# Optimization experiments

Measured on AMD Instinct MI355X. Metric: run time of the kernel, lower is better.

Reference implementation:

```python
import jax, jax.numpy as jnp
import numpy as np

B, T, C, H = 4, 2048, 1024, 16
D = C // H


def setup_inputs() -> dict:
    key = jax.random.key(0)
    ks = jax.random.split(key, 5)
    s = C ** -0.5  # keep linear outputs O(1) like standard init
    x = jax.random.normal(ks[0], (B, T, C), dtype=jnp.float32)
    Wq = jax.random.normal(ks[1], (C, C), dtype=jnp.float32) * s
    Wk = jax.random.normal(ks[2], (C, C), dtype=jnp.float32) * s
    Wv = jax.random.normal(ks[3], (C, C), dtype=jnp.float32) * s
    Wproj = jax.random.normal(ks[4], (C, C), dtype=jnp.float32) * s
    alpha_raw = jnp.zeros((1, H, 1, 1), dtype=jnp.float32)
    beta_raw = jnp.zeros((1, H, 1, 1), dtype=jnp.float32)
    state = jnp.zeros((B, H, D, D), dtype=jnp.float32)
    return dict(x=x, Wq=Wq, Wk=Wk, Wv=Wv, Wproj=Wproj,
                alpha_raw=alpha_raw, beta_raw=beta_raw, state=state)


def reference(x, Wq, Wk, Wv, Wproj, alpha_raw, beta_raw, state):
    Bx, Tx, Cx = x.shape
    Hn = alpha_raw.shape[1]
    Dh = Cx // Hn
    # projections (torch Linear: x @ W^T), split heads -> (B, H, T, D)
    def proj(W):
        return (x @ W.T).reshape(Bx, Tx, Hn, Dh).transpose(0, 2, 1, 3)
    q, k, v = proj(Wq), proj(Wk), proj(Wv)
    # F.normalize(k, dim=-1) with eps=1e-12
    k = k / jnp.maximum(jnp.linalg.norm(k, axis=-1, keepdims=True), 1e-12)
    alpha = jax.nn.sigmoid(alpha_raw) * 0.5  # (1, H, 1, 1)
    beta = jax.nn.sigmoid(beta_raw) * 0.5

    def step(st, qkv):
        qt, kt, vt = qkv  # each (B, H, D)
        # y_t = q_t @ state^T
        y = jnp.einsum('bhe,bhde->bhd', qt, st)
        # Mk = state @ k_t
        Mk = jnp.einsum('bhde,bhe->bhd', st, kt)
        st = st - alpha * jnp.einsum('bhd,bhe->bhde', Mk, kt) \
                + beta * jnp.einsum('bhd,bhe->bhde', vt, kt)
        return st, y

    # scan over time: (T, B, H, D)
    qT = q.transpose(2, 0, 1, 3)
    kT = k.transpose(2, 0, 1, 3)
    vT = v.transpose(2, 0, 1, 3)
    state_f, ys = jax.lax.scan(step, state, (qT, kT, vT))
    y = ys.transpose(1, 0, 2, 3).reshape(Bx, Tx, Cx)  # (B, T, C)
    out = y @ Wproj.T
    return out, state_f
```

## Files before the change

kernel.cpp:

```cpp
#include <hip/hip_runtime.h>
#include <hip/hip_bf16.h>
#include <cstdint>

#define B_ 4
#define T_ 2048
#define C_ 1024
#define H_ 16
#define D_ 64
#define NC_ 32
#define L_ 64

typedef __attribute__((ext_vector_type(8))) short bf16x8;
typedef __attribute__((ext_vector_type(4))) float f32x4;

static __device__ __forceinline__ unsigned short f2bf(float f) {
  unsigned u = __float_as_uint(f);
  u += 0x7fff + ((u >> 16) & 1);
  return (unsigned short)(u >> 16);
}
static __device__ __forceinline__ float bf2f(unsigned short b) {
  return __uint_as_float(((unsigned)b) << 16);
}
static __device__ __forceinline__ int swz128(int row, int byte) {
  return row * 128 + (byte ^ ((row & 7) << 4));
}

#define LDS_BARRIER() asm volatile("s_waitcnt lgkmcnt(0)\ns_barrier" ::: "memory")

__global__ __launch_bounds__(256) void cvt_kernel(const float* __restrict__ src,
                                                  unsigned short* __restrict__ dst, int n) {
  int i = (blockIdx.x * 256 + threadIdx.x) * 4;
  if (i >= n) return;
  float4 v = *reinterpret_cast<const float4*>(src + i);
  ushort4 o;
  o.x = f2bf(v.x); o.y = f2bf(v.y); o.z = f2bf(v.z); o.w = f2bf(v.w);
  *reinterpret_cast<ushort4*>(dst + i) = o;
}

__global__ __launch_bounds__(256) void cvt_w_kernel(const float* __restrict__ wq,
                                                    const float* __restrict__ wk,
                                                    const float* __restrict__ wv,
                                                    const float* __restrict__ wp,
                                                    unsigned short* __restrict__ W3,
                                                    unsigned short* __restrict__ Wp) {
  const int g = blockIdx.x >> 10;
  const float* src = (g == 0) ? wq : (g == 1) ? wk : (g == 2) ? wv : wp;
  unsigned short* dst = (g < 3) ? (W3 + (long)g * 1048576) : Wp;
  int i = ((blockIdx.x & 1023) * 256 + threadIdx.x) * 4;
  float4 v = *reinterpret_cast<const float4*>(src + i);
  ushort4 o;
  o.x = f2bf(v.x); o.y = f2bf(v.y); o.z = f2bf(v.z); o.w = f2bf(v.w);
  *reinterpret_cast<ushort4*>(dst + i) = o;
}

#define STAGE256(GP, GR0, KT, LOFF) do {                                          \
    const unsigned short* _s = (GP) + ((GR0) + wid * 8 + lr8) * 1024L             \
                               + (long)(KT) * 64 + skb * 8;                       \
    char* _d = (char*)lds + (LOFF) + wid * 1024;                                  \
    __builtin_amdgcn_global_load_lds((const __attribute__((address_space(1))) void*)_s,      \
        (__attribute__((address_space(3))) void*)_d, 16, 0, 0);                   \
    __builtin_amdgcn_global_load_lds((const __attribute__((address_space(1))) void*)(_s + 64 * 1024L), \
        (__attribute__((address_space(3))) void*)(_d + 8192), 16, 0, 0);          \
  } while (0)

#define PHASE256(AO, BO, MH, NH, STG) do {                                        \
    asm volatile("s_waitcnt vmcnt(6)" ::: "memory");                              \
    bf16x8 av[4][2], bv[2][2];                                                    \
    {                                                                             \
      const char* ab = (const char*)lds + (AO) + (MH) * 16384 + arow;             \
      const char* bb = (const char*)lds + (BO) + (NH) * 16384 + brow;             \
      _Pragma("unroll")                                                           \
      for (int j = 0; j < 4; ++j) {                                               \
        av[j][0] = *(const bf16x8*)(ab + j * 4096 + cb0);                         \
        av[j][1] = *(const bf16x8*)(ab + j * 4096 + cb1);                         \
      }                                                                           \
      _Pragma("unroll")                                                           \
      for (int j2 = 0; j2 < 2; ++j2) {                                            \
        bv[j2][0] = *(const bf16x8*)(bb + j2 * 8192 + cb0);                       \
        bv[j2][1] = *(const bf16x8*)(bb + j2 * 8192 + cb1);                       \
      }                                                                           \
    }                                                                             \
    STG;                                                                          \
    __builtin_amdgcn_s_barrier();                                                 \
    asm volatile("s_waitcnt lgkmcnt(0)" ::: "memory");                            \
    __builtin_amdgcn_sched_barrier(0);                                            \
    __builtin_amdgcn_s_setprio(1);                                                \
    _Pragma("unroll")                                                             \
    for (int j = 0; j < 4; ++j)                                                   \
      _Pragma("unroll")                                                           \
      for (int j2 = 0; j2 < 2; ++j2)                                              \
        acc[(MH) * 4 + j][(NH) * 2 + j2] = __builtin_amdgcn_mfma_f32_16x16x32_bf16( \
            av[j][0], bv[j2][0], acc[(MH) * 4 + j][(NH) * 2 + j2], 0, 0, 0);      \
    _Pragma("unroll")                                                             \
    for (int j = 0; j < 4; ++j)                                                   \
      _Pragma("unroll")                                                           \
      for (int j2 = 0; j2 < 2; ++j2)                                              \
        acc[(MH) * 4 + j][(NH) * 2 + j2] = __builtin_amdgcn_mfma_f32_16x16x32_bf16( \
            av[j][1], bv[j2][1], acc[(MH) * 4 + j][(NH) * 2 + j2], 0, 0, 0);      \
    __builtin_amdgcn_s_setprio(0);                                                \
    __builtin_amdgcn_s_barrier();                                                 \
  } while (0)

__global__ __launch_bounds__(512, 2) void gemm256_bt(
    const unsigned short* __restrict__ A,
    const unsigned short* __restrict__ Bw,
    unsigned short* __restrict__ C, int N) {
  __shared__ __align__(16) char lds[131072];
  enum { EA = 0, EB = 32768, OA = 65536, OB = 98304, HF = 16384 };
  const int tid = threadIdx.x;
  const int wid = tid >> 6, lane = tid & 63;
  const int wm = wid >> 2, wn = wid & 3;
  const int f = lane & 15, g = lane >> 4;
  const int lr8 = lane >> 3, lc = lane & 7;
  const int skb = lc ^ lr8;
  const int bid = blockIdx.y * gridDim.x + blockIdx.x;
  const int cpx = (gridDim.x * gridDim.y) >> 3;
  const int sw = (bid & 7) * cpx + (bid >> 3);
  const long bM = (long)(sw / gridDim.x) * 256;
  const long bN = (long)(sw % gridDim.x) * 256;
  const int cb0 = ((0 + g) ^ (f & 7)) * 16;
  const int cb1 = ((4 + g) ^ (f & 7)) * 16;
  const int arow = (wm * 16 + f) * 128;
  const int brow = (wn * 16 + f) * 128;

  f32x4 acc[8][4] = {};

  STAGE256(A, bM, 0, EA);
  STAGE256(Bw, bN, 0, EB);
  STAGE256(A, bM + 128, 0, EA + HF);
  STAGE256(Bw, bN + 128, 0, EB + HF);
  STAGE256(Bw, bN, 1, OB);
  STAGE256(A, bM, 1, OA);
  asm volatile("s_waitcnt vmcnt(8)" ::: "memory");
  __builtin_amdgcn_s_barrier();

  for (int i = 0; i < 8; ++i) {
    const int todd = 2 * i + 1;
    int te = 2 * i + 2; if (te > 14) te = 14;
    int to = 2 * i + 3; if (to > 15) to = 15;
    PHASE256(EA, EB, 0, 0, STAGE256(A, bM + 128, todd, OA + HF));
    PHASE256(EA, EB, 1, 0, STAGE256(Bw, bN + 128, todd, OB + HF));
    PHASE256(EA, EB, 0, 1, STAGE256(Bw, bN, te, EB));
    PHASE256(EA, EB, 1, 1, STAGE256(A, bM, te, EA));
    PHASE256(OA, OB, 0, 0, STAGE256(A, bM + 128, te, EA + HF));
    PHASE256(OA, OB, 1, 0, STAGE256(Bw, bN + 128, te, EB + HF));
    PHASE256(OA, OB, 0, 1, STAGE256(Bw, bN, to, OB));
    PHASE256(OA, OB, 1, 1, STAGE256(A, bM, to, OA));
  }

#pragma unroll
  for (int mf = 0; mf < 8; ++mf) {
    long row = bM + (mf >> 2) * 128 + (mf & 3) * 32 + wm * 16 + g * 4;
#pragma unroll
    for (int nf = 0; nf < 4; ++nf) {
      long col = bN + (nf >> 1) * 128 + (nf & 1) * 64 + wn * 16 + f;
#pragma unroll
      for (int r = 0; r < 4; ++r)
        C[(row + r) * (long)N + col] = f2bf(acc[mf][nf][r]);
    }
  }
}

template<int OUT_BF16>
__global__ __launch_bounds__(256) void gemm_bt(const unsigned short* __restrict__ A,
                                               const unsigned short* __restrict__ Bw,
                                               void* __restrict__ Cp,
                                               int M, int N, int K) {
  __shared__ __align__(16) unsigned short sA[128 * 32];
  __shared__ __align__(16) unsigned short sB[128 * 32];
  const int tid = threadIdx.x;
  const int wid = tid >> 6, lane = tid & 63;
  const int wm = wid >> 1, wn = wid & 1;
  const int bid = blockIdx.y * gridDim.x + blockIdx.x;
  const int cpx = (gridDim.x * gridDim.y) >> 3;
  const int sw = (bid & 7) * cpx + (bid >> 3);
  const long blockM = (long)(sw / gridDim.x) * 128;
  const long blockN = (long)(sw % gridDim.x) * 128;

  f32x4 acc[4][4] = {};

  const int ar = lane >> 2;
  const int ac = (lane & 3) * 8;
  const unsigned short* Abase = A + (blockM + wid * 32 + ar) * (long)K + ac;
  const unsigned short* Bbase = Bw + (blockN + wid * 32 + ar) * (long)K + ac;
  char* sAb = (char*)sA + wid * 2048;
  char* sBb = (char*)sB + wid * 2048;

  for (int k0 = 0; k0 < K; k0 += 32) {
    __syncthreads();
    __builtin_amdgcn_global_load_lds((const __attribute__((address_space(1))) void*)(Abase + k0),
                                     (__attribute__((address_space(3))) void*)(sAb), 16, 0, 0);
    __builtin_amdgcn_global_load_lds((const __attribute__((address_space(1))) void*)(Abase + 16 * (long)K + k0),
                                     (__attribute__((address_space(3))) void*)(sAb + 1024), 16, 0, 0);
    __builtin_amdgcn_global_load_lds((const __attribute__((address_space(1))) void*)(Bbase + k0),
                                     (__attribute__((address_space(3))) void*)(sBb), 16, 0, 0);
    __builtin_amdgcn_global_load_lds((const __attribute__((address_space(1))) void*)(Bbase + 16 * (long)K + k0),
                                     (__attribute__((address_space(3))) void*)(sBb + 1024), 16, 0, 0);
    __syncthreads();

    const int koff = (lane >> 4) * 8;
    const int rA = wm * 64 + (lane & 15);
    const int rB = wn * 64 + (lane & 15);
    bf16x8 af[4], bfr[4];
#pragma unroll
    for (int m = 0; m < 4; ++m)
      af[m] = *reinterpret_cast<const bf16x8*>(&sA[(rA + m * 16) * 32 + koff]);
#pragma unroll
    for (int n = 0; n < 4; ++n)
      bfr[n] = *reinterpret_cast<const bf16x8*>(&sB[(rB + n * 16) * 32 + koff]);
#pragma unroll
    for (int m = 0; m < 4; ++m)
#pragma unroll
      for (int n = 0; n < 4; ++n)
        acc[m][n] = __builtin_amdgcn_mfma_f32_16x16x32_bf16(af[m], bfr[n], acc[m][n], 0, 0, 0);
  }

  const int cr = (lane >> 4) * 4;
  const int cc = lane & 15;
#pragma unroll
  for (int m = 0; m < 4; ++m) {
    long R = blockM + wm * 64 + m * 16 + cr;
#pragma unroll
    for (int n = 0; n < 4; ++n) {
      long Cc = blockN + wn * 64 + n * 16 + cc;
#pragma unroll
      for (int r = 0; r < 4; ++r) {
        if (OUT_BF16)
          ((unsigned short*)Cp)[(R + r) * (long)N + Cc] = f2bf(acc[m][n][r]);
        else
          ((float*)Cp)[(R + r) * (long)N + Cc] = acc[m][n][r];
      }
    }
  }
}

__global__ __launch_bounds__(256) void chunk_prep(
    unsigned short* __restrict__ qkv,
    const float* __restrict__ a_raw, const float* __restrict__ b_raw,
    unsigned short* __restrict__ Ubuf, unsigned short* __restrict__ Wbuf,
    unsigned short* __restrict__ SLbuf) {
  __shared__ __align__(16) unsigned short sK[64 * 64];
  __shared__ __align__(16) unsigned short sQ[64 * 64];
  __shared__ __align__(16) unsigned short sV[64 * 64];
  __shared__ float sA[64 * 64];

  const int blk = blockIdx.x;
  const int bh = blk >> 5, c = blk & 31;
  const int b = bh >> 4, h = bh & 15;
  const int tid = threadIdx.x;
  const int wid = tid >> 6, lane = tid & 63;

  const float alpha = 0.5f / (1.f + __expf(-a_raw[h]));
  const float beta  = 0.5f / (1.f + __expf(-b_raw[h]));

  {
    const int row = tid >> 2, cg = tid & 3;
    unsigned short* gp = qkv + (long)(b * 2048 + c * 64 + row) * 3072 + h * 64 + cg * 16;
    bf16x8 q0 = *(const bf16x8*)(gp);
    bf16x8 q1 = *(const bf16x8*)(gp + 8);
    bf16x8 k0 = *(const bf16x8*)(gp + 1024);
    bf16x8 k1 = *(const bf16x8*)(gp + 1024 + 8);
    bf16x8 v0 = *(const bf16x8*)(gp + 2048);
    bf16x8 v1 = *(const bf16x8*)(gp + 2048 + 8);
    float kf[16];
    float ss = 0.f;
#pragma unroll
    for (int i = 0; i < 8; ++i) { kf[i] = bf2f((unsigned short)k0[i]); ss += kf[i] * kf[i]; }
#pragma unroll
    for (int i = 0; i < 8; ++i) { kf[8 + i] = bf2f((unsigned short)k1[i]); ss += kf[8 + i] * kf[8 + i]; }
    ss += __shfl_xor(ss, 1);
    ss += __shfl_xor(ss, 2);
    const float inv = 1.f / fmaxf(sqrtf(ss), 1e-12f);
    bf16x8 n0, n1;
#pragma unroll
    for (int i = 0; i < 8; ++i) { n0[i] = (short)f2bf(kf[i] * inv); n1[i] = (short)f2bf(kf[8 + i] * inv); }
    *(bf16x8*)((char*)sK + swz128(row, cg * 32)) = n0;
    *(bf16x8*)((char*)sK + swz128(row, cg * 32 + 16)) = n1;
    *(bf16x8*)((char*)sQ + swz128(row, cg * 32)) = q0;
    *(bf16x8*)((char*)sQ + swz128(row, cg * 32 + 16)) = q1;
    *(bf16x8*)((char*)sV + row * 128 + cg * 32) = v0;
    *(bf16x8*)((char*)sV + row * 128 + cg * 32 + 16) = v1;
  }
  __syncthreads();

  {
    const int erow = tid >> 2, tq = tid & 3;
    unsigned short kt[16];
#pragma unroll
    for (int i = 0; i < 16; ++i)
      kt[i] = *(const unsigned short*)((const char*)sK + swz128(tq * 16 + i, 2 * erow));
    unsigned short* vp = qkv + (long)(b * 2048 + c * 64 + erow) * 3072 + 2048 + h * 64 + tq * 16;
    *(bf16x8*)vp = *(const bf16x8*)kt;
    *(bf16x8*)(vp + 8) = *(const bf16x8*)(kt + 8);
  }

  const int rfrag = lane & 15, koff = (lane >> 4) * 8, crow = (lane >> 4) * 4;
  const int w2 = wid & 1;
  if (wid < 2) {
#pragma unroll
    for (int mt = 0; mt < 2; ++mt) {
      const int m = w2 * 2 + mt;
      const int ra = 16 * m + rfrag;
      f32x4 acc[4] = {};
#pragma unroll
      for (int ks = 0; ks < 2; ++ks) {
        bf16x8 af = *(const bf16x8*)((const char*)sK + swz128(ra, ks * 64 + koff * 2));
#pragma unroll
        for (int n = 0; n < 4; ++n) {
          bf16x8 bf = *(const bf16x8*)((const char*)sK + swz128(16 * n + rfrag, ks * 64 + koff * 2));
          acc[n] = __builtin_amdgcn_mfma_f32_16x16x32_bf16(af, bf, acc[n], 0, 0, 0);
        }
      }
#pragma unroll
      for (int n = 0; n < 4; ++n)
#pragma unroll
        for (int r = 0; r < 4; ++r)
          sA[(16 * m + crow + r) * 64 + 16 * n + rfrag] = acc[n][r];
    }
  } else {
#pragma unroll
    for (int mt = 0; mt < 2; ++mt) {
      const int m = w2 * 2 + mt;
      const int ra = 16 * m + rfrag;
      f32x4 acc[4] = {};
#pragma unroll
      for (int ks = 0; ks < 2; ++ks) {
        bf16x8 af = *(const bf16x8*)((const char*)sQ + swz128(ra, ks * 64 + koff * 2));
#pragma unroll
        for (int n = 0; n < 4; ++n) {
          bf16x8 bf = *(const bf16x8*)((const char*)sK + swz128(16 * n + rfrag, ks * 64 + koff * 2));
          acc[n] = __builtin_amdgcn_mfma_f32_16x16x32_bf16(af, bf, acc[n], 0, 0, 0);
        }
      }
#pragma unroll
      for (int n = 0; n < 4; ++n)
#pragma unroll
        for (int r = 0; r < 4; ++r) {
          int t = 16 * m + crow + r, j = 16 * n + rfrag;
          SLbuf[(long)blk * 4096 + t * 64 + j] = (j < t) ? f2bf(acc[n][r]) : (unsigned short)0;
        }
    }
  }
  __syncthreads();

  if (wid < 2) {
    const int d = lane;
    float x[64];
#pragma unroll
    for (int t = 0; t < 64; ++t) {
      float rhs;
      if (wid == 0) rhs = beta * bf2f(sV[t * 64 + d]);
      else          rhs = alpha * bf2f(*(const unsigned short*)((const char*)sK + swz128(t, 2 * d)));
      float s = 0.f;
#pragma unroll
      for (int j = 0; j < t; ++j) s = fmaf(sA[t * 64 + j], x[j], s);
      x[t] = rhs - alpha * s;
    }
    unsigned short* ob = (wid == 0 ? Ubuf : Wbuf) + (long)blk * 4096 + d;
#pragma unroll
    for (int t = 0; t < 64; ++t) ob[t * 64] = f2bf(x[t]);
  }
}

__global__ __launch_bounds__(256) void chunk_scan(
    const unsigned short* __restrict__ qkv,
    const unsigned short* __restrict__ Ubuf, const unsigned short* __restrict__ Wbuf,
    const unsigned short* __restrict__ SLbuf,
    const float* __restrict__ state_in, unsigned short* __restrict__ ybuf,
    float* __restrict__ state_out) {
  __shared__ __align__(16) unsigned short sQ[64 * 64];
  __shared__ __align__(16) unsigned short sW[64 * 64];
  __shared__ __align__(16) unsigned short sSL[64 * 64];
  __shared__ __align__(16) unsigned short sKT[64 * 64];
  __shared__ __align__(16) unsigned short sU[64 * 16];
  __shared__ __align__(16) unsigned short sGT[16 * 64];
  __shared__ __align__(16) unsigned short sS[16 * 64];

  const int bid0 = blockIdx.x;
  const int blk = (bid0 & 7) * 32 + (bid0 >> 3);
  const int bh = blk >> 2, dq = blk & 3;
  const int b = bh >> 4, h = bh & 15;
  const int tid = threadIdx.x, wid = tid >> 6, lane = tid & 63;
  const int rfrag = lane & 15, koff = (lane >> 4) * 8, crow = (lane >> 4) * 4;
  const int row = tid >> 2, cg = tid & 3;

  const unsigned short* gpb = qkv + (long)(b * 2048 + row) * 3072 + h * 64 + cg * 16;
  const long tbb = ((long)(bh * 32) * 64 + row) * 64 + cg * 16;
  const long ubb = ((long)(bh * 32) * 64 + (tid >> 1)) * 64 + dq * 16 + (tid & 1) * 8;

  bf16x8 qv0, qv1, kt0, kt1, wv0, wv1, sl0, sl1, uv;
  {
    qv0 = *(const bf16x8*)gpb;
    qv1 = *(const bf16x8*)(gpb + 8);
    kt0 = *(const bf16x8*)(gpb + 2048);
    kt1 = *(const bf16x8*)(gpb + 2048 + 8);
    wv0 = *(const bf16x8*)(Wbuf + tbb);
    wv1 = *(const bf16x8*)(Wbuf + tbb + 8);
    sl0 = *(const bf16x8*)(SLbuf + tbb);
    sl1 = *(const bf16x8*)(SLbuf + tbb + 8);
    uv = (tid < 128) ? *(const bf16x8*)(Ubuf + ubb) : bf16x8{};
  }

  f32x4 sacc;
#pragma unroll
  for (int r = 0; r < 4; ++r)
    sacc[r] = state_in[(long)bh * 4096 + (dq * 16 + crow + r) * 64 + 16 * wid + rfrag];
#pragma unroll
  for (int r = 0; r < 4; ++r)
    *(unsigned short*)((char*)sS + swz128(crow + r, 2 * (16 * wid + rfrag))) = f2bf(sacc[r]);

  for (int c = 0; c < NC_; ++c) {
    *(bf16x8*)((char*)sQ + swz128(row, cg * 32)) = qv0;
    *(bf16x8*)((char*)sQ + swz128(row, cg * 32 + 16)) = qv1;
    *(bf16x8*)((char*)sW + swz128(row, cg * 32)) = wv0;
    *(bf16x8*)((char*)sW + swz128(row, cg * 32 + 16)) = wv1;
    *(bf16x8*)((char*)sSL + swz128(row, cg * 32)) = sl0;
    *(bf16x8*)((char*)sSL + swz128(row, cg * 32 + 16)) = sl1;
    *(bf16x8*)((char*)sKT + swz128(row, cg * 32)) = kt0;
    *(bf16x8*)((char*)sKT + swz128(row, cg * 32 + 16)) = kt1;
    if (tid < 128) *(bf16x8*)((char*)sU + ((tid >> 1) * 16 + (tid & 1) * 8) * 2) = uv;

    {
      const int cn = (c + 1 < NC_) ? c + 1 : c;
      const unsigned short* gp = gpb + (long)cn * 64 * 3072;
      const long tb = tbb + (long)cn * 4096;
      qv0 = *(const bf16x8*)gp;
      qv1 = *(const bf16x8*)(gp + 8);
      kt0 = *(const bf16x8*)(gp + 2048);
      kt1 = *(const bf16x8*)(gp + 2048 + 8);
      wv0 = *(const bf16x8*)(Wbuf + tb);
      wv1 = *(const bf16x8*)(Wbuf + tb + 8);
      sl0 = *(const bf16x8*)(SLbuf + tb);
      sl1 = *(const bf16x8*)(SLbuf + tb + 8);
      if (tid < 128) uv = *(const bf16x8*)(Ubuf + ubb + (long)cn * 4096);
    }
    LDS_BARRIER();

    const int ta = 16 * wid + rfrag;
    f32x4 p = {};
    f32x4 yac = {};
#pragma unroll
    for (int ks = 0; ks < 2; ++ks) {
      bf16x8 afw = *(const bf16x8*)((const char*)sW + swz128(ta, ks * 64 + koff * 2));
      bf16x8 afq = *(const bf16x8*)((const char*)sQ + swz128(ta, ks * 64 + koff * 2));
      bf16x8 bS = *(const bf16x8*)((const char*)sS + swz128(rfrag, ks * 64 + koff * 2));
      p = __builtin_amdgcn_mfma_f32_16x16x32_bf16(afw, bS, p, 0, 0, 0);
      yac = __builtin_amdgcn_mfma_f32_16x16x32_bf16(afq, bS, yac, 0, 0, 0);
    }
#pragma unroll
    for (int r = 0; r < 4; ++r) {
      int t = 16 * wid + crow + r;
      float gg = bf2f(sU[t * 16 + rfrag]) - p[r];
      *(unsigned short*)((char*)sGT + swz128(rfrag, 2 * t)) = f2bf(gg);
    }
    LDS_BARRIER();

#pragma unroll
    for (int ks = 0; ks < 2; ++ks) {
      bf16x8 aSL = *(const bf16x8*)((const char*)sSL + swz128(ta, ks * 64 + koff * 2));
      bf16x8 bGT = *(const bf16x8*)((const char*)sGT + swz128(rfrag, ks * 64 + koff * 2));
      yac = __builtin_amdgcn_mfma_f32_16x16x32_bf16(aSL, bGT, yac, 0, 0, 0);
    }
#pragma unroll
    for (int r = 0; r < 4; ++r) {
      int t = 16 * wid + crow + r;
      ybuf[(long)(b * 2048 + c * 64 + t) * 1024 + h * 64 + dq * 16 + rfrag] = f2bf(yac[r]);
    }
#pragma unroll
    for (int ks = 0; ks < 2; ++ks) {
      bf16x8 aGT = *(const bf16x8*)((const char*)sGT + swz128(rfrag, ks * 64 + koff * 2));
      bf16x8 bKT = *(const bf16x8*)((const char*)sKT + swz128(16 * wid + rfrag, ks * 64 + koff * 2));
      sacc = __builtin_amdgcn_mfma_f32_16x16x32_bf16(aGT, bKT, sacc, 0, 0, 0);
    }
    LDS_BARRIER();

#pragma unroll
    for (int r = 0; r < 4; ++r)
      *(unsigned short*)((char*)sS + swz128(crow + r, 2 * (16 * wid + rfrag))) = f2bf(sacc[r]);
  }

#pragma unroll
  for (int r = 0; r < 4; ++r)
    state_out[(long)bh * 4096 + (dq * 16 + crow + r) * 64 + 16 * wid + rfrag] = sacc[r];
}

extern "C" void kernel_launch(void* const* d_in, const int* in_sizes, int n_in,
                              void* d_out, int out_size, void* d_ws, size_t ws_size,
                              hipStream_t stream) {
  (void)in_sizes; (void)n_in; (void)out_size; (void)ws_size;
  const float* x     = (const float*)d_in[0];
  const float* Wq    = (const float*)d_in[1];
  const float* Wk    = (const float*)d_in[2];
  const float* Wv    = (const float*)d_in[3];
  const float* Wproj = (const float*)d_in[4];
  const float* a_raw = (const float*)d_in[5];
  const float* b_raw = (const float*)d_in[6];
  const float* state = (const float*)d_in[7];

  char* ws = (char*)d_ws;
  unsigned short* xbf = (unsigned short*)ws;
  unsigned short* W3  = (unsigned short*)(ws + (16l << 20));
  unsigned short* Wp  = (unsigned short*)(ws + (22l << 20));
  unsigned short* qkv = (unsigned short*)(ws + (24l << 20));
  unsigned short* Ub  = (unsigned short*)(ws + (72l << 20));
  unsigned short* Wb  = (unsigned short*)(ws + (88l << 20));
  unsigned short* SLb = (unsigned short*)(ws + (104l << 20));
  float* out = (float*)d_out;
  float* state_out = out + (long)B_ * T_ * C_;

  cvt_kernel<<<dim3(8192), dim3(256), 0, stream>>>(x, xbf, 8388608);
  cvt_w_kernel<<<dim3(4096), dim3(256), 0, stream>>>(Wq, Wk, Wv, Wproj, W3, Wp);

  gemm256_bt<<<dim3(3072 / 256, 8192 / 256), dim3(512), 0, stream>>>(xbf, W3, qkv, 3072);

  chunk_prep<<<dim3(2048), dim3(256), 0, stream>>>(qkv, a_raw, b_raw, Ub, Wb, SLb);
  chunk_scan<<<dim3(256), dim3(256), 0, stream>>>(qkv, Ub, Wb, SLb, state, xbf, state_out);

  gemm_bt<0><<<dim3(1024 / 128, 8192 / 128), dim3(256), 0, stream>>>(xbf, Wp, (void*)out, 8192, 1024, 1024);
}
```

Measured before the change: 187.0 us.

## Double-buffer chunk_scan LDS tiles and merge conversion kernels into one launch

The per-chunk LDS tiles in chunk_scan are now double-buffered, so the next chunk's tiles are written into the alternate buffer while the current one is consumed. This cuts each chunk iteration from three barriers to two and moves the state-update MFMA before the y stores. The x and weight fp32-to-bf16 conversion kernels are also fused into a single launch to save one kernel launch. The cost is more LDS per block (72KB), which could limit occupancy, though the scan only launches 256 blocks.

```diff
diff --git a/kernel.cpp b/kernel.cpp
--- a/kernel.cpp
+++ b/kernel.cpp
@@ -27,26 +27,27 @@
 
 #define LDS_BARRIER() asm volatile("s_waitcnt lgkmcnt(0)\ns_barrier" ::: "memory")
 
-__global__ __launch_bounds__(256) void cvt_kernel(const float* __restrict__ src,
-                                                  unsigned short* __restrict__ dst, int n) {
-  int i = (blockIdx.x * 256 + threadIdx.x) * 4;
-  if (i >= n) return;
-  float4 v = *reinterpret_cast<const float4*>(src + i);
-  ushort4 o;
-  o.x = f2bf(v.x); o.y = f2bf(v.y); o.z = f2bf(v.z); o.w = f2bf(v.w);
-  *reinterpret_cast<ushort4*>(dst + i) = o;
-}
-
-__global__ __launch_bounds__(256) void cvt_w_kernel(const float* __restrict__ wq,
-                                                    const float* __restrict__ wk,
-                                                    const float* __restrict__ wv,
-                                                    const float* __restrict__ wp,
-                                                    unsigned short* __restrict__ W3,
-                                                    unsigned short* __restrict__ Wp) {
-  const int g = blockIdx.x >> 10;
-  const float* src = (g == 0) ? wq : (g == 1) ? wk : (g == 2) ? wv : wp;
-  unsigned short* dst = (g < 3) ? (W3 + (long)g * 1048576) : Wp;
-  int i = ((blockIdx.x & 1023) * 256 + threadIdx.x) * 4;
+__global__ __launch_bounds__(256) void cvt_all(const float* __restrict__ x,
+                                               const float* __restrict__ wq,
+                                               const float* __restrict__ wk,
+                                               const float* __restrict__ wv,
+                                               const float* __restrict__ wp,
+                                               unsigned short* __restrict__ xbf,
+                                               unsigned short* __restrict__ W3,
+                                               unsigned short* __restrict__ Wp) {
+  const int bidx = blockIdx.x;
+  const float* src;
+  unsigned short* dst;
+  long base;
+  if (bidx < 8192) {
+    src = x; dst = xbf; base = (long)bidx * 1024;
+  } else {
+    const int g = (bidx - 8192) >> 10;
+    src = (g == 0) ? wq : (g == 1) ? wk : (g == 2) ? wv : wp;
+    dst = (g < 3) ? (W3 + (long)g * 1048576) : Wp;
+    base = (long)((bidx - 8192) & 1023) * 1024;
+  }
+  long i = base + threadIdx.x * 4;
   float4 v = *reinterpret_cast<const float4*>(src + i);
   ushort4 o;
   o.x = f2bf(v.x); o.y = f2bf(v.y); o.z = f2bf(v.z); o.w = f2bf(v.w);
@@ -368,13 +369,7 @@
     const unsigned short* __restrict__ SLbuf,
     const float* __restrict__ state_in, unsigned short* __restrict__ ybuf,
     float* __restrict__ state_out) {
-  __shared__ __align__(16) unsigned short sQ[64 * 64];
-  __shared__ __align__(16) unsigned short sW[64 * 64];
-  __shared__ __align__(16) unsigned short sSL[64 * 64];
-  __shared__ __align__(16) unsigned short sKT[64 * 64];
-  __shared__ __align__(16) unsigned short sU[64 * 16];
-  __shared__ __align__(16) unsigned short sGT[16 * 64];
-  __shared__ __align__(16) unsigned short sS[16 * 64];
+  __shared__ __align__(16) char lds[73728];
 
   const int bid0 = blockIdx.x;
   const int blk = (bid0 & 7) * 32 + (bid0 >> 3);
@@ -384,22 +379,36 @@
   const int rfrag = lane & 15, koff = (lane >> 4) * 8, crow = (lane >> 4) * 4;
   const int row = tid >> 2, cg = tid & 3;
 
+  char* gt = lds + 69632;
+  char* ssb = lds + 71680;
+
   const unsigned short* gpb = qkv + (long)(b * 2048 + row) * 3072 + h * 64 + cg * 16;
   const long tbb = ((long)(bh * 32) * 64 + row) * 64 + cg * 16;
   const long ubb = ((long)(bh * 32) * 64 + (tid >> 1)) * 64 + dq * 16 + (tid & 1) * 8;
 
   bf16x8 qv0, qv1, kt0, kt1, wv0, wv1, sl0, sl1, uv;
-  {
-    qv0 = *(const bf16x8*)gpb;
-    qv1 = *(const bf16x8*)(gpb + 8);
-    kt0 = *(const bf16x8*)(gpb + 2048);
-    kt1 = *(const bf16x8*)(gpb + 2048 + 8);
-    wv0 = *(const bf16x8*)(Wbuf + tbb);
-    wv1 = *(const bf16x8*)(Wbuf + tbb + 8);
-    sl0 = *(const bf16x8*)(SLbuf + tbb);
-    sl1 = *(const bf16x8*)(SLbuf + tbb + 8);
-    uv = (tid < 128) ? *(const bf16x8*)(Ubuf + ubb) : bf16x8{};
-  }
+#define LOADREGS(CN) do {                                                       \
+    const unsigned short* gp = gpb + (long)(CN) * 64 * 3072;                    \
+    const long tb = tbb + (long)(CN) * 4096;                                    \
+    qv0 = *(const bf16x8*)gp;            qv1 = *(const bf16x8*)(gp + 8);        \
+    kt0 = *(const bf16x8*)(gp + 2048);   kt1 = *(const bf16x8*)(gp + 2048 + 8); \
+    wv0 = *(const bf16x8*)(Wbuf + tb);   wv1 = *(const bf16x8*)(Wbuf + tb + 8); \
+    sl0 = *(const bf16x8*)(SLbuf + tb);  sl1 = *(const bf16x8*)(SLbuf + tb + 8);\
+    if (tid < 128) uv = *(const bf16x8*)(Ubuf + ubb + (long)(CN) * 4096);       \
+  } while (0)
+
+#define WRITE_TILES(BUF) do {                                                   \
+    char* bp = lds + (BUF) * 34816;                                             \
+    *(bf16x8*)(bp + swz128(row, cg * 32)) = qv0;                                \
+    *(bf16x8*)(bp + swz128(row, cg * 32 + 16)) = qv1;                           \
+    *(bf16x8*)(bp + 8192 + swz128(row, cg * 32)) = wv0;                         \
+    *(bf16x8*)(bp + 8192 + swz128(row, cg * 32 + 16)) = wv1;                    \
+    *(bf16x8*)(bp + 16384 + swz128(row, cg * 32)) = sl0;                        \
+    *(bf16x8*)(bp + 16384 + swz128(row, cg * 32 + 16)) = sl1;                   \
+    *(bf16x8*)(bp + 24576 + swz128(row, cg * 32)) = kt0;                        \
+    *(bf16x8*)(bp + 24576 + swz128(row, cg * 32 + 16)) = kt1;                   \
+    if (tid < 128) *(bf16x8*)(bp + 32768 + ((tid >> 1) * 16 + (tid & 1) * 8) * 2) = uv; \
+  } while (0)
 
   f32x4 sacc;
 #pragma unroll
@@ -407,59 +416,47 @@
     sacc[r] = state_in[(long)bh * 4096 + (dq * 16 + crow + r) * 64 + 16 * wid + rfrag];
 #pragma unroll
   for (int r = 0; r < 4; ++r)
-    *(unsigned short*)((char*)sS + swz128(crow + r, 2 * (16 * wid + rfrag))) = f2bf(sacc[r]);
+    *(unsigned short*)(ssb + swz128(crow + r, 2 * (16 * wid + rfrag))) = f2bf(sacc[r]);
+
+  LOADREGS(0);
+  WRITE_TILES(0);
+  LOADREGS(1);
+  LDS_BARRIER();
 
   for (int c = 0; c < NC_; ++c) {
-    *(bf16x8*)((char*)sQ + swz128(row, cg * 32)) = qv0;
-    *(bf16x8*)((char*)sQ + swz128(row, cg * 32 + 16)) = qv1;
-    *(bf16x8*)((char*)sW + swz128(row, cg * 32)) = wv0;
-    *(bf16x8*)((char*)sW + swz128(row, cg * 32 + 16)) = wv1;
-    *(bf16x8*)((char*)sSL + swz128(row, cg * 32)) = sl0;
-    *(bf16x8*)((char*)sSL + swz128(row, cg * 32 + 16)) = sl1;
-    *(bf16x8*)((char*)sKT + swz128(row, cg * 32)) = kt0;
-    *(bf16x8*)((char*)sKT + swz128(row, cg * 32 + 16)) = kt1;
-    if (tid < 128) *(bf16x8*)((char*)sU + ((tid >> 1) * 16 + (tid & 1) * 8) * 2) = uv;
-
-    {
-      const int cn = (c + 1 < NC_) ? c + 1 : c;
-      const unsigned short* gp = gpb + (long)cn * 64 * 3072;
-      const long tb = tbb + (long)cn * 4096;
-      qv0 = *(const bf16x8*)gp;
-      qv1 = *(const bf16x8*)(gp + 8);
-      kt0 = *(const bf16x8*)(gp + 2048);
-      kt1 = *(const bf16x8*)(gp + 2048 + 8);
-      wv0 = *(const bf16x8*)(Wbuf + tb);
-      wv1 = *(const bf16x8*)(Wbuf + tb + 8);
-      sl0 = *(const bf16x8*)(SLbuf + tb);
-      sl1 = *(const bf16x8*)(SLbuf + tb + 8);
-      if (tid < 128) uv = *(const bf16x8*)(Ubuf + ubb + (long)cn * 4096);
-    }
-    LDS_BARRIER();
-
+    const int cur = c & 1;
+    const char* bp = lds + cur * 34816;
     const int ta = 16 * wid + rfrag;
+
     f32x4 p = {};
     f32x4 yac = {};
 #pragma unroll
     for (int ks = 0; ks < 2; ++ks) {
-      bf16x8 afw = *(const bf16x8*)((const char*)sW + swz128(ta, ks * 64 + koff * 2));
-      bf16x8 afq = *(const bf16x8*)((const char*)sQ + swz128(ta, ks * 64 + koff * 2));
-      bf16x8 bS = *(const bf16x8*)((const char*)sS + swz128(rfrag, ks * 64 + koff * 2));
+      bf16x8 afw = *(const bf16x8*)(bp + 8192 + swz128(ta, ks * 64 + koff * 2));
+      bf16x8 afq = *(const bf16x8*)(bp + swz128(ta, ks * 64 + koff * 2));
+      bf16x8 bS = *(const bf16x8*)(ssb + swz128(rfrag, ks * 64 + koff * 2));
       p = __builtin_amdgcn_mfma_f32_16x16x32_bf16(afw, bS, p, 0, 0, 0);
       yac = __builtin_amdgcn_mfma_f32_16x16x32_bf16(afq, bS, yac, 0, 0, 0);
     }
 #pragma unroll
     for (int r = 0; r < 4; ++r) {
       int t = 16 * wid + crow + r;
-      float gg = bf2f(sU[t * 16 + rfrag]) - p[r];
-      *(unsigned short*)((char*)sGT + swz128(rfrag, 2 * t)) = f2bf(gg);
+      float gg = bf2f(*(const unsigned short*)(bp + 32768 + (t * 16 + rfrag) * 2)) - p[r];
+      *(unsigned short*)(gt + swz128(rfrag, 2 * t)) = f2bf(gg);
     }
     LDS_BARRIER();
 
 #pragma unroll
     for (int ks = 0; ks < 2; ++ks) {
-      bf16x8 aSL = *(const bf16x8*)((const char*)sSL + swz128(ta, ks * 64 + koff * 2));
-      bf16x8 bGT = *(const bf16x8*)((const char*)sGT + swz128(rfrag, ks * 64 + koff * 2));
+      bf16x8 aSL = *(const bf16x8*)(bp + 16384 + swz128(ta, ks * 64 + koff * 2));
+      bf16x8 bGT = *(const bf16x8*)(gt + swz128(rfrag, ks * 64 + koff * 2));
       yac = __builtin_amdgcn_mfma_f32_16x16x32_bf16(aSL, bGT, yac, 0, 0, 0);
+    }
+#pragma unroll
+    for (int ks = 0; ks < 2; ++ks) {
+      bf16x8 aGT = *(const bf16x8*)(gt + swz128(rfrag, ks * 64 + koff * 2));
+      bf16x8 bKT = *(const bf16x8*)(bp + 24576 + swz128(16 * wid + rfrag, ks * 64 + koff * 2));
+      sacc = __builtin_amdgcn_mfma_f32_16x16x32_bf16(aGT, bKT, sacc, 0, 0, 0);
     }
 #pragma unroll
     for (int r = 0; r < 4; ++r) {
@@ -467,21 +464,21 @@
       ybuf[(long)(b * 2048 + c * 64 + t) * 1024 + h * 64 + dq * 16 + rfrag] = f2bf(yac[r]);
     }
 #pragma unroll
-    for (int ks = 0; ks < 2; ++ks) {
-      bf16x8 aGT = *(const bf16x8*)((const char*)sGT + swz128(rfrag, ks * 64 + koff * 2));
-      bf16x8 bKT = *(const bf16x8*)((const char*)sKT + swz128(16 * wid + rfrag, ks * 64 + koff * 2));
-      sacc = __builtin_amdgcn_mfma_f32_16x16x32_bf16(aGT, bKT, sacc, 0, 0, 0);
+    for (int r = 0; r < 4; ++r)
+      *(unsigned short*)(ssb + swz128(crow + r, 2 * (16 * wid + rfrag))) = f2bf(sacc[r]);
+    if (c + 1 < NC_) {
+      WRITE_TILES(cur ^ 1);
+      int cn = c + 2; if (cn > NC_ - 1) cn = NC_ - 1;
+      LOADREGS(cn);
     }
     LDS_BARRIER();
-
-#pragma unroll
-    for (int r = 0; r < 4; ++r)
-      *(unsigned short*)((char*)sS + swz128(crow + r, 2 * (16 * wid + rfrag))) = f2bf(sacc[r]);
   }
 
 #pragma unroll
   for (int r = 0; r < 4; ++r)
     state_out[(long)bh * 4096 + (dq * 16 + crow + r) * 64 + 16 * wid + rfrag] = sacc[r];
+#undef LOADREGS
+#undef WRITE_TILES
 }
 
 extern "C" void kernel_launch(void* const* d_in, const int* in_sizes, int n_in,
@@ -508,8 +505,7 @@
   float* out = (float*)d_out;
   float* state_out = out + (long)B_ * T_ * C_;
 
-  cvt_kernel<<<dim3(8192), dim3(256), 0, stream>>>(x, xbf, 8388608);
-  cvt_w_kernel<<<dim3(4096), dim3(256), 0, stream>>>(Wq, Wk, Wv, Wproj, W3, Wp);
+  cvt_all<<<dim3(12288), dim3(256), 0, stream>>>(x, Wq, Wk, Wv, Wproj, xbf, W3, Wp);
 
   gemm256_bt<<<dim3(3072 / 256, 8192 / 256), dim3(512), 0, stream>>>(xbf, W3, qkv, 3072);
 
```

Measured after the change: 180.8 us. 1.03x faster.
